# Kernel optimization log

Hardware: AMD Instinct MI355X
Metric: run time of the kernel (lower is better)

## Reference

```python
import jax, jax.numpy as jnp
import numpy as np

B, CIN, H, W = 4, 64, 128, 128
COUT, K, S, P = 64, 3, 1, 1


def setup_inputs() -> dict:
    key = jax.random.key(0)
    k1, k2, k3, k4 = jax.random.split(key, 4)
    x = jax.random.normal(k1, (B, CIN, H, W), jnp.float32)
    # offset-predicting conv params (small scale so offsets stay in a sane range)
    offset_w = jax.random.normal(k2, (2 * K * K, CIN, K, K), jnp.float32) * 0.01
    offset_b = jnp.zeros((2 * K * K,), jnp.float32)
    # deformable conv params
    fan_in = CIN * K * K
    deform_w = jax.random.normal(k3, (COUT, CIN, K, K), jnp.float32) / np.sqrt(fan_in).astype(np.float32)
    deform_b = jax.random.normal(k4, (COUT,), jnp.float32) * 0.01
    return {"x": x, "offset_w": offset_w, "offset_b": offset_b,
            "deform_w": deform_w, "deform_b": deform_b}


def _conv2d(x, w, b, stride, pad):
    y = jax.lax.conv_general_dilated(
        x, w, window_strides=(stride, stride),
        padding=[(pad, pad), (pad, pad)],
        dimension_numbers=("NCHW", "OIHW", "NCHW"))
    return y + b[None, :, None, None]


def _deform_conv2d(x, offset, w, b, stride, pad):
    Bn, C, Hi, Wi = x.shape
    O, _, Kh, Kw = w.shape
    KK = Kh * Kw
    Ho = (Hi + 2 * pad - Kh) // stride + 1
    Wo = (Wi + 2 * pad - Kw) // stride + 1
    # offset layout (torchvision/mmcv): [B, KK, 2, Ho, Wo] with (dy, dx)
    off = offset.reshape(Bn, KK, 2, Ho, Wo)
    dy, dx = off[:, :, 0], off[:, :, 1]
    ky, kx = jnp.meshgrid(jnp.arange(Kh), jnp.arange(Kw), indexing="ij")
    ky = ky.reshape(-1).astype(x.dtype)  # [KK]
    kx = kx.reshape(-1).astype(x.dtype)
    hgrid = (jnp.arange(Ho) * stride - pad).astype(x.dtype)  # [Ho]
    wgrid = (jnp.arange(Wo) * stride - pad).astype(x.dtype)  # [Wo]
    # fractional sampling coords [B, KK, Ho, Wo]
    ys = hgrid[None, None, :, None] + ky[None, :, None, None] + dy
    xs = wgrid[None, None, None, :] + kx[None, :, None, None] + dx
    y0 = jnp.floor(ys)
    x0 = jnp.floor(xs)
    ly = (ys - y0)[:, None]  # [B,1,KK,Ho,Wo] for channel broadcast
    lx = (xs - x0)[:, None]
    y0i = y0.astype(jnp.int32)
    x0i = x0.astype(jnp.int32)

    def samp(yi, xi):
        valid = (yi >= 0) & (yi < Hi) & (xi >= 0) & (xi < Wi)
        yc = jnp.clip(yi, 0, Hi - 1)
        xc = jnp.clip(xi, 0, Wi - 1)
        # per-batch gather -> [B, C, KK, Ho, Wo]
        v = jax.vmap(lambda im, yy, xx: im[:, yy, xx])(x, yc, xc)
        return v * valid[:, None].astype(x.dtype)

    v00 = samp(y0i, x0i)
    v01 = samp(y0i, x0i + 1)
    v10 = samp(y0i + 1, x0i)
    v11 = samp(y0i + 1, x0i + 1)
    sampled = (v00 * (1 - ly) * (1 - lx) + v01 * (1 - ly) * lx
               + v10 * ly * (1 - lx) + v11 * ly * lx)  # [B,C,KK,Ho,Wo]
    out = jnp.einsum("bckhw,ock->bohw", sampled, w.reshape(O, C, KK))
    return out + b[None, :, None, None]


def reference(x, offset_w, offset_b, deform_w, deform_b):
    offset = _conv2d(x, offset_w, offset_b, S, P)
    return _deform_conv2d(x, offset, deform_w, deform_b, S, P)
```

## Files before the change

kernel.cpp:

```cpp
#include <hip/hip_runtime.h>
#include <hip/hip_bf16.h>

#define B_    4
#define CIN_  64
#define H_    128
#define W_    128
#define COUT_ 64
#define KK_   9
#define OFFC_ 18
#define HW_   (H_*W_)
#define TILE_ 64

typedef _Float16 hf8 __attribute__((ext_vector_type(8)));
typedef float f32x4  __attribute__((ext_vector_type(4)));

__device__ inline _Float16 f2h(float f) { return (_Float16)f; }

__global__ __launch_bounds__(256) void prep_all(
    const float* __restrict__ x,
    const float* __restrict__ ow, const float* __restrict__ dw,
    _Float16* __restrict__ xt, _Float16* __restrict__ dwh, _Float16* __restrict__ owh)
{
    const int tid = threadIdx.x;
    const int bid = blockIdx.x;
    if (bid < 1024) {
        const int b  = bid >> 8;
        const int pb = bid & 255;
        const int p  = tid & 63;
        const int g  = tid >> 6;
        const int pix = pb * 64 + p;
        const float* src = x + ((size_t)b * CIN_ + g * 16) * HW_ + pix;
        _Float16 vals[16];
        #pragma unroll
        for (int j = 0; j < 16; ++j) vals[j] = f2h(src[(size_t)j * HW_]);
        _Float16* dst = xt + ((size_t)b * HW_ + pix) * 64 + g * 16;
        *(hf8*)dst       = *(hf8*)&vals[0];
        *(hf8*)(dst + 8) = *(hf8*)&vals[8];
    } else {
        const int idx = (bid - 1024) * 256 + tid;
        {
            const int k = idx / (COUT_ * CIN_);
            const int r = idx % (COUT_ * CIN_);
            const int o = r >> 6, c = r & 63;
            dwh[idx] = f2h(dw[(o * CIN_ + c) * KK_ + k]);
        }
        if (idx < KK_ * 32 * CIN_) {
            const int k = idx / (32 * CIN_);
            const int r = idx % (32 * CIN_);
            const int co = r >> 6, c = r & 63;
            owh[idx] = f2h(co < OFFC_ ? ow[(co * CIN_ + c) * KK_ + k] : 0.0f);
        }
    }
}

#define DECL_SET(S) \
    hf8 r00a##S, r00b##S, r01a##S, r01b##S, r10a##S, r10b##S, r11a##S, r11b##S; \
    float pm0##S, pm1##S, pm2##S, pm3##S;

#define LOAD_SET(S, t) { \
    const int ky = (t) / 3, kx = (t) % 3; \
    const float dy = offs[(2 * (t) + 0) * TILE_ + p]; \
    const float dx = offs[(2 * (t) + 1) * TILE_ + p]; \
    const float ys = (float)(ho + ky - 1) + dy; \
    const float xs = (float)(wo + kx - 1) + dx; \
    const float y0f = floorf(ys), x0f = floorf(xs); \
    const float ly = ys - y0f, lx = xs - x0f; \
    const int y0 = (int)y0f, x0 = (int)x0f; \
    const int y1 = y0 + 1,   x1 = x0 + 1; \
    const bool y0v = (y0 >= 0) & (y0 < H_); \
    const bool y1v = (y1 >= 0) & (y1 < H_); \
    const bool x0v = (x0 >= 0) & (x0 < W_); \
    const bool x1v = (x1 >= 0) & (x1 < W_); \
    pm0##S = (y0v & x0v) ? (1.f - ly) * (1.f - lx) : 0.f; \
    pm1##S = (y0v & x1v) ? (1.f - ly) * lx         : 0.f; \
    pm2##S = (y1v & x0v) ? ly * (1.f - lx)         : 0.f; \
    pm3##S = (y1v & x1v) ? ly * lx                 : 0.f; \
    const int y0c = min(max(y0, 0), H_ - 1); \
    const int y1c = min(max(y1, 0), H_ - 1); \
    const int x0c = min(max(x0, 0), W_ - 1); \
    const int x1c = min(max(x1, 0), W_ - 1); \
    const _Float16* c00 = xbt + (size_t)(y0c * W_ + x0c) * 64 + sub * 8; \
    const _Float16* c01 = xbt + (size_t)(y0c * W_ + x1c) * 64 + sub * 8; \
    const _Float16* c10 = xbt + (size_t)(y1c * W_ + x0c) * 64 + sub * 8; \
    const _Float16* c11 = xbt + (size_t)(y1c * W_ + x1c) * 64 + sub * 8; \
    r00a##S = *(const hf8*)(c00); r00b##S = *(const hf8*)(c00 + 32); \
    r01a##S = *(const hf8*)(c01); r01b##S = *(const hf8*)(c01 + 32); \
    r10a##S = *(const hf8*)(c10); r10b##S = *(const hf8*)(c10 + 32); \
    r11a##S = *(const hf8*)(c11); r11b##S = *(const hf8*)(c11 + 32); \
}

#define COMBINE_WRITE(S, dstbuf) { \
    const hf8 m00v = (hf8)f2h(pm0##S); \
    const hf8 m01v = (hf8)f2h(pm1##S); \
    const hf8 m10v = (hf8)f2h(pm2##S); \
    const hf8 m11v = (hf8)f2h(pm3##S); \
    const hf8 va = m00v * r00a##S + m01v * r01a##S + m10v * r10a##S + m11v * r11a##S; \
    const hf8 vb = m00v * r00b##S + m01v * r01b##S + m10v * r10b##S + m11v * r11b##S; \
    const int cA = sub; \
    const int cB = sub + 4; \
    *(hf8*)&u.smp[(dstbuf) * 4096 + p * 64 + ((cA ^ (p & 7)) << 3)] = va; \
    *(hf8*)&u.smp[(dstbuf) * 4096 + p * 64 + ((cB ^ (p & 7)) << 3)] = vb; \
}

__global__ __launch_bounds__(256, 4) void fused_deform_mfma(
    const _Float16* __restrict__ xt,
    const _Float16* __restrict__ owh,
    const float* __restrict__ obias,
    const _Float16* __restrict__ dwh,
    const float* __restrict__ dbias,
    float* __restrict__ out)
{
    __shared__ union {
        _Float16 xtl[3 * 66 * 64];
        _Float16 smp[4 * 64 * 64];
    } u;
    __shared__ float offs[OFFC_ * TILE_];

    const int lin  = blockIdx.x;
    const int nid  = (lin & 7) * 128 + (lin >> 3);
    const int b    = nid >> 8;
    const int tile = nid & 255;

    const int tid = threadIdx.x;
    const int pixbase = tile * TILE_;
    const int ho    = pixbase >> 7;
    const int wbase = pixbase & (W_ - 1);
    const int lane  = tid & 63;
    const int wv    = tid >> 6;
    const int arow  = lane & 15;
    const int kseg  = lane >> 4;

    const _Float16* xbt = xt + (size_t)b * HW_ * 64;

    for (int base = 0; base < 3 * 66 * 8; base += 256) {
        const int idx = base + tid;
        if (idx < 3 * 66 * 8) {
            const int cc = idx & 7;
            const int qy = idx >> 3;
            const int y  = qy / 66;
            const int q  = qy - y * 66;
            const int gy = ho + y - 1;
            const int gx = wbase + q - 1;
            hf8 v;
            if (gy >= 0 && gy < H_ && gx >= 0 && gx < W_) {
                v = *(const hf8*)&xbt[(size_t)(gy * W_ + gx) * 64 + cc * 8];
            } else {
                v = (hf8)(_Float16)0.0f;
            }
            *(hf8*)&u.xtl[(y * 66 + q) * 64 + ((cc ^ (q & 7)) << 3)] = v;
        }
    }
    __syncthreads();

    {
        const int m = wv & 1;
        const int h = wv >> 1;
        f32x4 acca[2];
        acca[0] = (f32x4)0.f; acca[1] = (f32x4)0.f;
        for (int t = 0; t < KK_; ++t) {
            const int ky = t / 3, kx = t % 3;
            #pragma unroll
            for (int kc = 0; kc < 2; ++kc) {
                const int cbase = kc * 32 + kseg * 8;
                const hf8 afrag = *(const hf8*)&owh[(t * 32 + m * 16 + arow) * 64 + cbase];
                const int cchunk = cbase >> 3;
                #pragma unroll
                for (int nt = 0; nt < 2; ++nt) {
                    const int pp = h * 32 + nt * 16 + arow;
                    const int q = pp + kx;
                    const hf8 bfrag = *(const hf8*)&u.xtl[(ky * 66 + q) * 64 + ((cchunk ^ (q & 7)) << 3)];
                    acca[nt] = __builtin_amdgcn_mfma_f32_16x16x32_f16(afrag, bfrag, acca[nt], 0, 0, 0);
                }
            }
        }
        #pragma unroll
        for (int nt = 0; nt < 2; ++nt) {
            #pragma unroll
            for (int r = 0; r < 4; ++r) {
                const int co = m * 16 + kseg * 4 + r;
                if (co < OFFC_) {
                    const int pp = h * 32 + nt * 16 + arow;
                    offs[co * TILE_ + pp] = acca[nt][r] + obias[co];
                }
            }
        }
    }
    __syncthreads();

    const int pix16 = lane >> 2;
    const int sub   = lane & 3;
    const int p     = wv * 16 + pix16;
    const int wo    = wbase + p;

    DECL_SET(A)
    DECL_SET(B)

    f32x4 accb[4];
    #pragma unroll
    for (int nt = 0; nt < 4; ++nt) accb[nt] = (f32x4)0.f;

    auto mfmaTap = [&](int t, int srcbuf) {
        #pragma unroll
        for (int kc = 0; kc < 2; ++kc) {
            const int cbase = kc * 32 + kseg * 8;
            const hf8 afrag = *(const hf8*)&dwh[(t * 64 + wv * 16 + arow) * 64 + cbase];
            const int cchunk = cbase >> 3;
            #pragma unroll
            for (int nt = 0; nt < 4; ++nt) {
                const int pp = nt * 16 + arow;
                const hf8 bfrag = *(const hf8*)&u.smp[srcbuf * 4096 + pp * 64 + ((cchunk ^ (pp & 7)) << 3)];
                accb[nt] = __builtin_amdgcn_mfma_f32_16x16x32_f16(afrag, bfrag, accb[nt], 0, 0, 0);
            }
        }
    };

    LOAD_SET(A, 0)
    LOAD_SET(B, 1)
    COMBINE_WRITE(A, 0)
    COMBINE_WRITE(B, 1)
    __syncthreads();

    #pragma unroll
    for (int r = 0; r < 4; ++r) {
        const int ta = 2 * r + 2;
        const int tb = 2 * r + 3;
        const int sb = ((r + 1) & 1) * 2;
        const int cb = (r & 1) * 2;
        LOAD_SET(A, ta)
        if (tb < KK_) LOAD_SET(B, tb)
        mfmaTap(2 * r,     cb + 0);
        mfmaTap(2 * r + 1, cb + 1);
        COMBINE_WRITE(A, sb + 0)
        if (tb < KK_) COMBINE_WRITE(B, sb + 1)
        __syncthreads();
    }
    mfmaTap(8, 0);

    float* ob = out + (size_t)b * COUT_ * HW_ + pixbase;
    #pragma unroll
    for (int nt = 0; nt < 4; ++nt) {
        const int pp = nt * 16 + arow;
        #pragma unroll
        for (int r = 0; r < 4; ++r) {
            const int o = wv * 16 + kseg * 4 + r;
            ob[(size_t)o * HW_ + pp] = accb[nt][r] + dbias[o];
        }
    }
}

extern "C" void kernel_launch(void* const* d_in, const int* in_sizes, int n_in,
                              void* d_out, int out_size, void* d_ws, size_t ws_size,
                              hipStream_t stream) {
    const float* x        = (const float*)d_in[0];
    const float* offset_w = (const float*)d_in[1];
    const float* offset_b = (const float*)d_in[2];
    const float* deform_w = (const float*)d_in[3];
    const float* deform_b = (const float*)d_in[4];
    float* out = (float*)d_out;

    _Float16* dwh = (_Float16*)d_ws;
    _Float16* owh = (_Float16*)((char*)d_ws + 73728);
    _Float16* xt  = (_Float16*)((char*)d_ws + 110592);

    prep_all<<<1024 + 144, 256, 0, stream>>>(x, offset_w, deform_w, xt, dwh, owh);

    fused_deform_mfma<<<1024, 256, 0, stream>>>(xt, owh, offset_b, dwh, deform_b, out);
}
```

Before: 46.09 us.

## Halve pixel tile to 32 and double grid with 8 channel-chunks per pixel

```diff
diff --git a/kernel.cpp b/kernel.cpp
--- a/kernel.cpp
+++ b/kernel.cpp
@@ -9,7 +9,9 @@
 #define KK_   9
 #define OFFC_ 18
 #define HW_   (H_*W_)
-#define TILE_ 64
+#define TILE_ 32
+#define PW_   34
+#define SMPSZ (TILE_ * 64)
 
 typedef _Float16 hf8 __attribute__((ext_vector_type(8)));
 typedef float f32x4  __attribute__((ext_vector_type(4)));
@@ -54,7 +56,7 @@
 }
 
 #define DECL_SET(S) \
-    hf8 r00a##S, r00b##S, r01a##S, r01b##S, r10a##S, r10b##S, r11a##S, r11b##S; \
+    hf8 r00##S, r01##S, r10##S, r11##S; \
     float pm0##S, pm1##S, pm2##S, pm3##S;
 
 #define LOAD_SET(S, t) { \
@@ -79,14 +81,10 @@
     const int y1c = min(max(y1, 0), H_ - 1); \
     const int x0c = min(max(x0, 0), W_ - 1); \
     const int x1c = min(max(x1, 0), W_ - 1); \
-    const _Float16* c00 = xbt + (size_t)(y0c * W_ + x0c) * 64 + sub * 8; \
-    const _Float16* c01 = xbt + (size_t)(y0c * W_ + x1c) * 64 + sub * 8; \
-    const _Float16* c10 = xbt + (size_t)(y1c * W_ + x0c) * 64 + sub * 8; \
-    const _Float16* c11 = xbt + (size_t)(y1c * W_ + x1c) * 64 + sub * 8; \
-    r00a##S = *(const hf8*)(c00); r00b##S = *(const hf8*)(c00 + 32); \
-    r01a##S = *(const hf8*)(c01); r01b##S = *(const hf8*)(c01 + 32); \
-    r10a##S = *(const hf8*)(c10); r10b##S = *(const hf8*)(c10 + 32); \
-    r11a##S = *(const hf8*)(c11); r11b##S = *(const hf8*)(c11 + 32); \
+    r00##S = *(const hf8*)(xbt + (size_t)(y0c * W_ + x0c) * 64 + sub * 8); \
+    r01##S = *(const hf8*)(xbt + (size_t)(y0c * W_ + x1c) * 64 + sub * 8); \
+    r10##S = *(const hf8*)(xbt + (size_t)(y1c * W_ + x0c) * 64 + sub * 8); \
+    r11##S = *(const hf8*)(xbt + (size_t)(y1c * W_ + x1c) * 64 + sub * 8); \
 }
 
 #define COMBINE_WRITE(S, dstbuf) { \
@@ -94,12 +92,8 @@
     const hf8 m01v = (hf8)f2h(pm1##S); \
     const hf8 m10v = (hf8)f2h(pm2##S); \
     const hf8 m11v = (hf8)f2h(pm3##S); \
-    const hf8 va = m00v * r00a##S + m01v * r01a##S + m10v * r10a##S + m11v * r11a##S; \
-    const hf8 vb = m00v * r00b##S + m01v * r01b##S + m10v * r10b##S + m11v * r11b##S; \
-    const int cA = sub; \
-    const int cB = sub + 4; \
-    *(hf8*)&u.smp[(dstbuf) * 4096 + p * 64 + ((cA ^ (p & 7)) << 3)] = va; \
-    *(hf8*)&u.smp[(dstbuf) * 4096 + p * 64 + ((cB ^ (p & 7)) << 3)] = vb; \
+    const hf8 va = m00v * r00##S + m01v * r01##S + m10v * r10##S + m11v * r11##S; \
+    *(hf8*)&u.smp[(dstbuf) * SMPSZ + p * 64 + ((sub ^ (p & 7)) << 3)] = va; \
 }
 
 __global__ __launch_bounds__(256, 4) void fused_deform_mfma(
@@ -111,15 +105,15 @@
     float* __restrict__ out)
 {
     __shared__ union {
-        _Float16 xtl[3 * 66 * 64];
-        _Float16 smp[4 * 64 * 64];
+        _Float16 xtl[3 * PW_ * 64];
+        _Float16 smp[4 * SMPSZ];
     } u;
     __shared__ float offs[OFFC_ * TILE_];
 
     const int lin  = blockIdx.x;
-    const int nid  = (lin & 7) * 128 + (lin >> 3);
-    const int b    = nid >> 8;
-    const int tile = nid & 255;
+    const int nid  = (lin & 7) * 256 + (lin >> 3);
+    const int b    = nid >> 9;
+    const int tile = nid & 511;
 
     const int tid = threadIdx.x;
     const int pixbase = tile * TILE_;
@@ -132,13 +126,13 @@
 
     const _Float16* xbt = xt + (size_t)b * HW_ * 64;
 
-    for (int base = 0; base < 3 * 66 * 8; base += 256) {
+    for (int base = 0; base < 3 * PW_ * 8; base += 256) {
         const int idx = base + tid;
-        if (idx < 3 * 66 * 8) {
+        if (idx < 3 * PW_ * 8) {
             const int cc = idx & 7;
             const int qy = idx >> 3;
-            const int y  = qy / 66;
-            const int q  = qy - y * 66;
+            const int y  = qy / PW_;
+            const int q  = qy - y * PW_;
             const int gy = ho + y - 1;
             const int gx = wbase + q - 1;
             hf8 v;
@@ -147,7 +141,7 @@
             } else {
                 v = (hf8)(_Float16)0.0f;
             }
-            *(hf8*)&u.xtl[(y * 66 + q) * 64 + ((cc ^ (q & 7)) << 3)] = v;
+            *(hf8*)&u.xtl[(y * PW_ + q) * 64 + ((cc ^ (q & 7)) << 3)] = v;
         }
     }
     __syncthreads();
@@ -155,49 +149,37 @@
     {
         const int m = wv & 1;
         const int h = wv >> 1;
-        f32x4 acca[2];
-        acca[0] = (f32x4)0.f; acca[1] = (f32x4)0.f;
+        const int pp = h * 16 + arow;
+        f32x4 acca = (f32x4)0.f;
         for (int t = 0; t < KK_; ++t) {
             const int ky = t / 3, kx = t % 3;
+            const int q  = pp + kx;
             #pragma unroll
             for (int kc = 0; kc < 2; ++kc) {
                 const int cbase = kc * 32 + kseg * 8;
                 const hf8 afrag = *(const hf8*)&owh[(t * 32 + m * 16 + arow) * 64 + cbase];
                 const int cchunk = cbase >> 3;
-                #pragma unroll
-                for (int nt = 0; nt < 2; ++nt) {
-                    const int pp = h * 32 + nt * 16 + arow;
-                    const int q = pp + kx;
-                    const hf8 bfrag = *(const hf8*)&u.xtl[(ky * 66 + q) * 64 + ((cchunk ^ (q & 7)) << 3)];
-                    acca[nt] = __builtin_amdgcn_mfma_f32_16x16x32_f16(afrag, bfrag, acca[nt], 0, 0, 0);
-                }
+                const hf8 bfrag = *(const hf8*)&u.xtl[(ky * PW_ + q) * 64 + ((cchunk ^ (q & 7)) << 3)];
+                acca = __builtin_amdgcn_mfma_f32_16x16x32_f16(afrag, bfrag, acca, 0, 0, 0);
             }
         }
         #pragma unroll
-        for (int nt = 0; nt < 2; ++nt) {
-            #pragma unroll
-            for (int r = 0; r < 4; ++r) {
-                const int co = m * 16 + kseg * 4 + r;
-                if (co < OFFC_) {
-                    const int pp = h * 32 + nt * 16 + arow;
-                    offs[co * TILE_ + pp] = acca[nt][r] + obias[co];
-                }
-            }
+        for (int r = 0; r < 4; ++r) {
+            const int co = m * 16 + kseg * 4 + r;
+            if (co < OFFC_) offs[co * TILE_ + pp] = acca[r] + obias[co];
         }
     }
     __syncthreads();
 
-    const int pix16 = lane >> 2;
-    const int sub   = lane & 3;
-    const int p     = wv * 16 + pix16;
-    const int wo    = wbase + p;
+    const int p   = tid >> 3;
+    const int sub = tid & 7;
+    const int wo  = wbase + p;
 
     DECL_SET(A)
     DECL_SET(B)
 
-    f32x4 accb[4];
-    #pragma unroll
-    for (int nt = 0; nt < 4; ++nt) accb[nt] = (f32x4)0.f;
+    f32x4 accb[2];
+    accb[0] = (f32x4)0.f; accb[1] = (f32x4)0.f;
 
     auto mfmaTap = [&](int t, int srcbuf) {
         #pragma unroll
@@ -206,9 +188,9 @@
             const hf8 afrag = *(const hf8*)&dwh[(t * 64 + wv * 16 + arow) * 64 + cbase];
             const int cchunk = cbase >> 3;
             #pragma unroll
-            for (int nt = 0; nt < 4; ++nt) {
+            for (int nt = 0; nt < 2; ++nt) {
                 const int pp = nt * 16 + arow;
-                const hf8 bfrag = *(const hf8*)&u.smp[srcbuf * 4096 + pp * 64 + ((cchunk ^ (pp & 7)) << 3)];
+                const hf8 bfrag = *(const hf8*)&u.smp[srcbuf * SMPSZ + pp * 64 + ((cchunk ^ (pp & 7)) << 3)];
                 accb[nt] = __builtin_amdgcn_mfma_f32_16x16x32_f16(afrag, bfrag, accb[nt], 0, 0, 0);
             }
         }
@@ -238,7 +220,7 @@
 
     float* ob = out + (size_t)b * COUT_ * HW_ + pixbase;
     #pragma unroll
-    for (int nt = 0; nt < 4; ++nt) {
+    for (int nt = 0; nt < 2; ++nt) {
         const int pp = nt * 16 + arow;
         #pragma unroll
         for (int r = 0; r < 4; ++r) {
@@ -264,5 +246,5 @@
 
     prep_all<<<1024 + 144, 256, 0, stream>>>(x, offset_w, deform_w, xt, dwh, owh);
 
-    fused_deform_mfma<<<1024, 256, 0, stream>>>(xt, owh, offset_b, dwh, deform_b, out);
-}
+    fused_deform_mfma<<<2048, 256, 0, stream>>>(xt, owh, offset_b, dwh, deform_b, out);
+}
```

Measured after the change: 65.56 us. +42.2%, slower.

## Precompute all tap sample addresses and weights; redirect invalid taps to zero pad

Applied to the files above, without the earlier changes.

```diff
diff --git a/kernel.cpp b/kernel.cpp
--- a/kernel.cpp
+++ b/kernel.cpp
@@ -10,6 +10,7 @@
 #define OFFC_ 18
 #define HW_   (H_*W_)
 #define TILE_ 64
+#define ZOFF  (B_ * HW_ * 64)
 
 typedef _Float16 hf8 __attribute__((ext_vector_type(8)));
 typedef float f32x4  __attribute__((ext_vector_type(4)));
@@ -37,6 +38,7 @@
         *(hf8*)dst       = *(hf8*)&vals[0];
         *(hf8*)(dst + 8) = *(hf8*)&vals[8];
     } else {
+        if (bid == 1024 && tid < 64) xt[(size_t)ZOFF + tid] = (_Float16)0.0f;
         const int idx = (bid - 1024) * 256 + tid;
         {
             const int k = idx / (COUT_ * CIN_);
@@ -54,46 +56,20 @@
 }
 
 #define DECL_SET(S) \
-    hf8 r00a##S, r00b##S, r01a##S, r01b##S, r10a##S, r10b##S, r11a##S, r11b##S; \
-    float pm0##S, pm1##S, pm2##S, pm3##S;
+    hf8 r00a##S, r00b##S, r01a##S, r01b##S, r10a##S, r10b##S, r11a##S, r11b##S;
 
 #define LOAD_SET(S, t) { \
-    const int ky = (t) / 3, kx = (t) % 3; \
-    const float dy = offs[(2 * (t) + 0) * TILE_ + p]; \
-    const float dx = offs[(2 * (t) + 1) * TILE_ + p]; \
-    const float ys = (float)(ho + ky - 1) + dy; \
-    const float xs = (float)(wo + kx - 1) + dx; \
-    const float y0f = floorf(ys), x0f = floorf(xs); \
-    const float ly = ys - y0f, lx = xs - x0f; \
-    const int y0 = (int)y0f, x0 = (int)x0f; \
-    const int y1 = y0 + 1,   x1 = x0 + 1; \
-    const bool y0v = (y0 >= 0) & (y0 < H_); \
-    const bool y1v = (y1 >= 0) & (y1 < H_); \
-    const bool x0v = (x0 >= 0) & (x0 < W_); \
-    const bool x1v = (x1 >= 0) & (x1 < W_); \
-    pm0##S = (y0v & x0v) ? (1.f - ly) * (1.f - lx) : 0.f; \
-    pm1##S = (y0v & x1v) ? (1.f - ly) * lx         : 0.f; \
-    pm2##S = (y1v & x0v) ? ly * (1.f - lx)         : 0.f; \
-    pm3##S = (y1v & x1v) ? ly * lx                 : 0.f; \
-    const int y0c = min(max(y0, 0), H_ - 1); \
-    const int y1c = min(max(y1, 0), H_ - 1); \
-    const int x0c = min(max(x0, 0), W_ - 1); \
-    const int x1c = min(max(x1, 0), W_ - 1); \
-    const _Float16* c00 = xbt + (size_t)(y0c * W_ + x0c) * 64 + sub * 8; \
-    const _Float16* c01 = xbt + (size_t)(y0c * W_ + x1c) * 64 + sub * 8; \
-    const _Float16* c10 = xbt + (size_t)(y1c * W_ + x0c) * 64 + sub * 8; \
-    const _Float16* c11 = xbt + (size_t)(y1c * W_ + x1c) * 64 + sub * 8; \
-    r00a##S = *(const hf8*)(c00); r00b##S = *(const hf8*)(c00 + 32); \
-    r01a##S = *(const hf8*)(c01); r01b##S = *(const hf8*)(c01 + 32); \
-    r10a##S = *(const hf8*)(c10); r10b##S = *(const hf8*)(c10 + 32); \
-    r11a##S = *(const hf8*)(c11); r11b##S = *(const hf8*)(c11 + 32); \
-}
-
-#define COMBINE_WRITE(S, dstbuf) { \
-    const hf8 m00v = (hf8)f2h(pm0##S); \
-    const hf8 m01v = (hf8)f2h(pm1##S); \
-    const hf8 m10v = (hf8)f2h(pm2##S); \
-    const hf8 m11v = (hf8)f2h(pm3##S); \
+    r00a##S = *(const hf8*)(xt + adr[t][0]); r00b##S = *(const hf8*)(xt + adr[t][0] + 32); \
+    r01a##S = *(const hf8*)(xt + adr[t][1]); r01b##S = *(const hf8*)(xt + adr[t][1] + 32); \
+    r10a##S = *(const hf8*)(xt + adr[t][2]); r10b##S = *(const hf8*)(xt + adr[t][2] + 32); \
+    r11a##S = *(const hf8*)(xt + adr[t][3]); r11b##S = *(const hf8*)(xt + adr[t][3] + 32); \
+}
+
+#define COMBINE_WRITE(S, t, dstbuf) { \
+    const hf8 m00v = (hf8)f2h(pmv[t][0]); \
+    const hf8 m01v = (hf8)f2h(pmv[t][1]); \
+    const hf8 m10v = (hf8)f2h(pmv[t][2]); \
+    const hf8 m11v = (hf8)f2h(pmv[t][3]); \
     const hf8 va = m00v * r00a##S + m01v * r01a##S + m10v * r10a##S + m11v * r11a##S; \
     const hf8 vb = m00v * r00b##S + m01v * r01b##S + m10v * r10b##S + m11v * r11b##S; \
     const int cA = sub; \
@@ -102,7 +78,7 @@
     *(hf8*)&u.smp[(dstbuf) * 4096 + p * 64 + ((cB ^ (p & 7)) << 3)] = vb; \
 }
 
-__global__ __launch_bounds__(256, 4) void fused_deform_mfma(
+__global__ __launch_bounds__(256, 3) void fused_deform_mfma(
     const _Float16* __restrict__ xt,
     const _Float16* __restrict__ owh,
     const float* __restrict__ obias,
@@ -191,6 +167,39 @@
     const int sub   = lane & 3;
     const int p     = wv * 16 + pix16;
     const int wo    = wbase + p;
+    const int boff  = b * HW_ * 64 + sub * 8;
+
+    int   adr[KK_][4];
+    float pmv[KK_][4];
+    #pragma unroll
+    for (int t = 0; t < KK_; ++t) {
+        const int ky = t / 3, kx = t % 3;
+        const float dy = offs[(2 * t + 0) * TILE_ + p];
+        const float dx = offs[(2 * t + 1) * TILE_ + p];
+        const float ys = (float)(ho + ky - 1) + dy;
+        const float xs = (float)(wo + kx - 1) + dx;
+        const float y0f = floorf(ys), x0f = floorf(xs);
+        const float ly = ys - y0f, lx = xs - x0f;
+        const int y0 = (int)y0f, x0 = (int)x0f;
+        const int y1 = y0 + 1,   x1 = x0 + 1;
+        const bool y0v = (y0 >= 0) & (y0 < H_);
+        const bool y1v = (y1 >= 0) & (y1 < H_);
+        const bool x0v = (x0 >= 0) & (x0 < W_);
+        const bool x1v = (x1 >= 0) & (x1 < W_);
+        pmv[t][0] = (1.f - ly) * (1.f - lx);
+        pmv[t][1] = (1.f - ly) * lx;
+        pmv[t][2] = ly * (1.f - lx);
+        pmv[t][3] = ly * lx;
+        const int y0c = min(max(y0, 0), H_ - 1);
+        const int y1c = min(max(y1, 0), H_ - 1);
+        const int x0c = min(max(x0, 0), W_ - 1);
+        const int x1c = min(max(x1, 0), W_ - 1);
+        const int zo = ZOFF + sub * 8;
+        adr[t][0] = (y0v & x0v) ? boff + (y0c * W_ + x0c) * 64 : zo;
+        adr[t][1] = (y0v & x1v) ? boff + (y0c * W_ + x1c) * 64 : zo;
+        adr[t][2] = (y1v & x0v) ? boff + (y1c * W_ + x0c) * 64 : zo;
+        adr[t][3] = (y1v & x1v) ? boff + (y1c * W_ + x1c) * 64 : zo;
+    }
 
     DECL_SET(A)
     DECL_SET(B)
@@ -216,8 +225,8 @@
 
     LOAD_SET(A, 0)
     LOAD_SET(B, 1)
-    COMBINE_WRITE(A, 0)
-    COMBINE_WRITE(B, 1)
+    COMBINE_WRITE(A, 0, 0)
+    COMBINE_WRITE(B, 1, 1)
     __syncthreads();
 
     #pragma unroll
@@ -230,8 +239,8 @@
         if (tb < KK_) LOAD_SET(B, tb)
         mfmaTap(2 * r,     cb + 0);
         mfmaTap(2 * r + 1, cb + 1);
-        COMBINE_WRITE(A, sb + 0)
-        if (tb < KK_) COMBINE_WRITE(B, sb + 1)
+        COMBINE_WRITE(A, ta, sb + 0)
+        if (tb < KK_) COMBINE_WRITE(B, tb, sb + 1)
         __syncthreads();
     }
     mfmaTap(8, 0);
```

New measurement: 47.53 us. +3.1%, slower.
